# Kernel tuning notes

Hardware: AMD Instinct MI355X
Metric: run time of the kernel (lower is better)

Reference implementation:

```python
import jax, jax.numpy as jnp
import numpy as np

G = 8      # conv groups
NH = 8     # attention heads per group
B, HID, S = 4, 2048, 4096
OUT = 2048


def setup_inputs() -> dict:
    key = jax.random.key(0)
    k1, k2, k3 = jax.random.split(key, 3)
    dim = HID // G
    # xavier-uniform-like scales for conv1d(k=1) weights
    sc_qkv = (6.0 / (dim + 3 * HID // 1)) ** 0.5 * 0.5
    sc_pred = (6.0 / (dim + OUT)) ** 0.5 * 0.5
    return {
        "x": jax.random.normal(k1, (B, HID, S), dtype=jnp.float32),
        # torch weight [3*hid, dim, 1] -> per-group [G, 3*dim, dim]
        "w_qkv": jax.random.uniform(k2, (G, 3 * dim, dim), jnp.float32, -sc_qkv, sc_qkv),
        "b_qkv": jnp.zeros((G, 3 * dim), jnp.float32),
        # torch weight [out, dim, 1] -> per-group [G, out//G, dim]
        "w_pred": jax.random.uniform(k3, (G, OUT // G, dim), jnp.float32, -sc_pred, sc_pred),
        "b_pred": jnp.zeros((G, OUT // G), jnp.float32),
    }


def reference(x, w_qkv, b_qkv, w_pred, b_pred):
    Bb, Hd, Ss = x.shape
    dim = Hd // G
    dk = dim // NH
    # ConstantPad1d((0,1),0)
    xp = jnp.pad(x, ((0, 0), (0, 0), (0, 1)))            # [B, Hd, S+1]
    xg = xp.reshape(Bb, G, dim, Ss + 1)
    # grouped 1x1 conv: per-group GEMM dim -> 3*dim
    y = jnp.einsum('bgct,goc->bgot', xg, w_qkv) + b_qkv[None, :, :, None]
    y = y.reshape(Bb, G, dim, 3, Ss + 1)                 # qkv interleaved per channel
    q = y[..., 0, :-1]                                   # [B, G, dim, S]
    k = jnp.concatenate((y[..., 1, :-1], y[..., 1, 1:]), axis=1)  # [B, 2G, dim, S]
    v = jnp.concatenate((y[..., 2, :-1], y[..., 2, 1:]), axis=1)
    qr = q.reshape(Bb, G, NH, dk, Ss)
    kr = k.reshape(Bb, 2 * G, NH, dk, Ss)
    vr = v.reshape(Bb, 2 * G, NH, dk, Ss)
    # scores[b,n,s,g,e] = sum_d q[b,g,n,d,s] k[b,e,n,d,s] / sqrt(dk)
    scores = jnp.einsum('bgnds,bends->bnsge', qr, kr) * (dk ** -0.5)
    # normalized sigmoid over last axis (2G)
    z = jax.nn.sigmoid(scores)
    attn = z / (1e-9 + jnp.sum(z, axis=-1, keepdims=True))
    # out[b,g,n,d,s] = sum_e attn[b,n,s,g,e] v[b,e,n,d,s]
    out = jnp.einsum('bnsge,bends->bgnds', attn, vr).reshape(Bb, Hd, Ss)
    og = out.reshape(Bb, G, dim, Ss)
    pred = jnp.einsum('bgct,goc->bgot', og, w_pred) + b_pred[None, :, :, None]
    pred = pred.reshape(Bb, -1, Ss)                      # [B, OUT, S]
    attn_out = jnp.transpose(attn, (0, 1, 3, 4, 2))      # [B, NH, G, 2G, S]
    return pred, attn_out
```

## Files before the change

### kernel.cpp

```cpp
#include <hip/hip_runtime.h>
#include <math.h>

#define BQ   4
#define GQ   8
#define NHQ  8
#define SQ   4096


typedef __attribute__((ext_vector_type(8))) short short8;
typedef __attribute__((ext_vector_type(4))) float f32x4;

__device__ __forceinline__ unsigned short f2b(float f) {
    unsigned int u = __float_as_uint(f);
    unsigned int r = u + 0x7fffu + ((u >> 16) & 1u);
    return (unsigned short)(r >> 16);
}
__device__ __forceinline__ float b2f(unsigned short h) {
    return __uint_as_float(((unsigned int)h) << 16);
}
__device__ __forceinline__ void gll16(const void* g, void* l) {
    __builtin_amdgcn_global_load_lds((const __attribute__((address_space(1))) void*)g,
                                     (__attribute__((address_space(3))) void*)l, 16, 0, 0);
}

__global__ __launch_bounds__(256) void convert_x_k(const float* __restrict__ x,
    unsigned short* __restrict__ xhi, unsigned short* __restrict__ xlo)
{
    __shared__ float lds[64 * 65];
    const int tid = threadIdx.x;
    const int t0 = blockIdx.x << 6;
    const int c0 = blockIdx.y << 6;
    const int bg = blockIdx.z;
    const int hi16 = tid >> 4, lo16 = tid & 15;
    const float* xb = x + ((size_t)bg << 8) * SQ;
#pragma unroll
    for (int p = 0; p < 4; ++p) {
        int c = (p << 4) + hi16;
        const float4 v4 = *(const float4*)(xb + (size_t)(c0 + c) * SQ + t0 + (lo16 << 2));
        lds[((lo16 << 2) + 0) * 65 + c] = v4.x;
        lds[((lo16 << 2) + 1) * 65 + c] = v4.y;
        lds[((lo16 << 2) + 2) * 65 + c] = v4.z;
        lds[((lo16 << 2) + 3) * 65 + c] = v4.w;
    }
    __syncthreads();
#pragma unroll
    for (int p = 0; p < 4; ++p) {
        int t = (p << 4) + hi16;
        float f0 = lds[t * 65 + (lo16 << 2) + 0];
        float f1 = lds[t * 65 + (lo16 << 2) + 1];
        float f2 = lds[t * 65 + (lo16 << 2) + 2];
        float f3 = lds[t * 65 + (lo16 << 2) + 3];
        ushort4 h, l;
        h.x = f2b(f0); l.x = f2b(f0 - b2f(h.x));
        h.y = f2b(f1); l.y = f2b(f1 - b2f(h.y));
        h.z = f2b(f2); l.z = f2b(f2 - b2f(h.z));
        h.w = f2b(f3); l.w = f2b(f3 - b2f(h.w));
        size_t o = (((size_t)bg * SQ + t0 + t) << 8) + c0 + (lo16 << 2);
        *(ushort4*)(xhi + o) = h;
        *(ushort4*)(xlo + o) = l;
    }
}

template <int M, bool QKV>
__global__ __launch_bounds__(256) void gemm2_k(
    const float* __restrict__ W,
    const unsigned short* __restrict__ Bh, const unsigned short* __restrict__ Bl,
    const float* __restrict__ bias,
    float* __restrict__ o0p, float* __restrict__ o1p, float* __restrict__ o2p)
{
    __shared__ __align__(16) char smem[32768];
    const int AHI = 0, ALO = 8192, BHI = 16384, BLO = 24576;
    const int tid = threadIdx.x;
    const int lane = tid & 63, wid = tid >> 6;
    const int wm = wid >> 1, wn = wid & 1;
    const int o0 = blockIdx.x << 7;
    const int t0 = blockIdx.y << 7;
    const int bg = blockIdx.z;
    const int g = bg & 7;
    const float* Wg = W + (size_t)g * M * 256;
    const size_t brow0 = (((size_t)bg * SQ + t0) << 8);

    f32x4 acc[4][4];
    const f32x4 zero = {0.f, 0.f, 0.f, 0.f};
#pragma unroll
    for (int i = 0; i < 4; ++i)
#pragma unroll
        for (int j = 0; j < 4; ++j) acc[i][j] = zero;

    for (int k0 = 0; k0 < 256; k0 += 32) {
#pragma unroll
        for (int s = 0; s < 2; ++s) {
            int w = tid + (s << 8);
            int row = w >> 2;
            int j = (w & 3) ^ ((w >> 3) & 3);
            size_t go = brow0 + ((size_t)row << 8) + k0 + (j << 3);
            gll16(Bh + go, smem + BHI + (w << 4));
            gll16(Bl + go, smem + BLO + (w << 4));
        }
#pragma unroll
        for (int p = 0; p < 4; ++p) {
            int qd = tid + (p << 8);
            int row = qd >> 3, kq = qd & 7;
            const float4 a4 = *(const float4*)(Wg + (size_t)(o0 + row) * 256 + k0 + (kq << 2));
            ushort4 h, l;
            h.x = f2b(a4.x); l.x = f2b(a4.x - b2f(h.x));
            h.y = f2b(a4.y); l.y = f2b(a4.y - b2f(h.y));
            h.z = f2b(a4.z); l.z = f2b(a4.z - b2f(h.z));
            h.w = f2b(a4.w); l.w = f2b(a4.w - b2f(h.w));
            int base = (row << 6) + ((((kq >> 1) ^ ((row >> 1) & 3)) << 4)) + ((kq & 1) << 3);
            *(ushort4*)(smem + AHI + base) = h;
            *(ushort4*)(smem + ALO + base) = l;
        }
        __syncthreads();

        short8 ah[4], al[4], bh[4], bl[4];
        const int lr = lane & 15, kc = lane >> 4;
#pragma unroll
        for (int mi = 0; mi < 4; ++mi) {
            int row = (wm << 6) + (mi << 4) + lr;
            int off = (row << 6) + ((kc ^ ((row >> 1) & 3)) << 4);
            ah[mi] = *(const short8*)(smem + AHI + off);
            al[mi] = *(const short8*)(smem + ALO + off);
        }
#pragma unroll
        for (int ni = 0; ni < 4; ++ni) {
            int row = (wn << 6) + (ni << 4) + lr;
            int off = (row << 6) + ((kc ^ ((row >> 1) & 3)) << 4);
            bh[ni] = *(const short8*)(smem + BHI + off);
            bl[ni] = *(const short8*)(smem + BLO + off);
        }
#pragma unroll
        for (int mi = 0; mi < 4; ++mi)
#pragma unroll
            for (int ni = 0; ni < 4; ++ni)
                acc[mi][ni] = __builtin_amdgcn_mfma_f32_16x16x32_bf16(ah[mi], bh[ni], acc[mi][ni], 0, 0, 0);
#pragma unroll
        for (int mi = 0; mi < 4; ++mi)
#pragma unroll
            for (int ni = 0; ni < 4; ++ni)
                acc[mi][ni] = __builtin_amdgcn_mfma_f32_16x16x32_bf16(ah[mi], bl[ni], acc[mi][ni], 0, 0, 0);
#pragma unroll
        for (int mi = 0; mi < 4; ++mi)
#pragma unroll
            for (int ni = 0; ni < 4; ++ni)
                acc[mi][ni] = __builtin_amdgcn_mfma_f32_16x16x32_bf16(al[mi], bh[ni], acc[mi][ni], 0, 0, 0);
        __syncthreads();
    }

    const int lr = lane & 15, lq = lane >> 4;
#pragma unroll
    for (int mi = 0; mi < 4; ++mi) {
#pragma unroll
        for (int r = 0; r < 4; ++r) {
            const int row = o0 + (wm << 6) + (mi << 4) + (lq << 2) + r;
            const float bo = bias[g * M + row];
            float* rowbase;
            if (QKV) {
                const int j = row % 3, c = row / 3;
                float* bp = (j == 0) ? o0p : ((j == 1) ? o1p : o2p);
                rowbase = bp + (((size_t)bg * 256 + c) << 12);
            } else {
                rowbase = o0p + (((size_t)(bg >> 3) * 2048 + g * 256 + row) << 12);
            }
#pragma unroll
            for (int ni = 0; ni < 4; ++ni) {
                const int t = t0 + (wn << 6) + (ni << 4) + lr;
                rowbase[t] = acc[mi][ni][r] + bo;
            }
        }
    }
}

__global__ __launch_bounds__(256) void pad_k(const float* __restrict__ bqkv,
                                             float* __restrict__ kpad, float* __restrict__ vpad)
{
    int i = blockIdx.x * 256 + threadIdx.x;
    int c = i & 255;
    int g = (i >> 8) & 7;
    kpad[i] = bqkv[g * 768 + c * 3 + 1];
    vpad[i] = bqkv[g * 768 + c * 3 + 2];
}

__global__ __launch_bounds__(256) void attn_k(
    const float* __restrict__ q, const float* __restrict__ k, const float* __restrict__ v,
    const float* __restrict__ kpad, const float* __restrict__ vpad,
    unsigned short* __restrict__ oghi, unsigned short* __restrict__ oglo,
    float* __restrict__ aout)
{
    __shared__ float qo_s[4620];
    __shared__ float k_s[4607];
    __shared__ float v_s[4607];
    __shared__ float at_s[2182];

    const int tid = threadIdx.x;
    const int t0 = blockIdx.x << 4;
    const int n  = blockIdx.y;
    const int b  = blockIdx.z;

#pragma unroll
    for (int i = 0; i < 4; ++i) {
        int f = tid + (i << 8);
        int row = f >> 2, cq = f & 3;
        int d = row >> 3, g = row & 7;
        const float4 val = *(const float4*)(q + (((size_t)((b * GQ + g) * 256 + n * 32 + d)) << 12) + t0 + (cq << 2));
        float* lp = &qo_s[row * 18 + (cq << 2)];
        lp[0] = val.x; lp[1] = val.y; lp[2] = val.z; lp[3] = val.w;
    }
#pragma unroll
    for (int i = 0; i < 4; ++i) {
        int f = tid + (i << 8);
        int r = f >> 2, cq = f & 3;
        int d = r >> 3, e8 = r & 7;
        size_t gofs = (((size_t)((b * GQ + e8) * 256 + n * 32 + d)) << 12) + t0 + (cq << 2);
        const float4 k4 = *(const float4*)(k + gofs);
        float* lk = &k_s[(d * 8 + e8) * 18 + (cq << 2)];
        lk[0] = k4.x; lk[1] = k4.y; lk[2] = k4.z; lk[3] = k4.w;
        const float4 v4 = *(const float4*)(v + gofs);
        float* lv = &v_s[(e8 * 32 + d) * 18 + (cq << 2)];
        lv[0] = v4.x; lv[1] = v4.y; lv[2] = v4.z; lv[3] = v4.w;
    }
    {
        int r = tid;
        int d = r >> 3, e8 = r & 7;
        float kv, vv;
        if (t0 + 16 < SQ) {
            size_t gofs = (((size_t)((b * GQ + e8) * 256 + n * 32 + d)) << 12) + t0 + 16;
            kv = k[gofs]; vv = v[gofs];
        } else {
            int pi = (b * GQ + e8) * 256 + n * 32 + d;
            kv = kpad[pi]; vv = vpad[pi];
        }
        k_s[(d * 8 + e8) * 18 + 16] = kv;
        v_s[(e8 * 32 + d) * 18 + 16] = vv;
    }
    __syncthreads();

    {
        const int p = tid >> 7;
        const int idx = tid & 127;
        const int g = idx >> 4, e = idx & 15;
        const int e8 = e & 7, hi = e >> 3;
#pragma unroll
        for (int it = 0; it < 8; ++it) {
            const int t = (it << 1) + p;
            float s = 0.f;
#pragma unroll
            for (int d = 0; d < 32; ++d)
                s += qo_s[(d * 8 + g) * 18 + t] * k_s[(d * 8 + e8) * 18 + t + hi];
            s *= 0.17677669529663687f;
            const float z = 1.f / (1.f + __expf(-s));
            float zs = z;
#pragma unroll
            for (int off = 1; off < 16; off <<= 1)
                zs += __shfl_xor(zs, off);
            at_s[(g * 16 + e) * 17 + g + t] = z / (1e-9f + zs);
        }
    }
    __syncthreads();

    {
        const int p4 = tid >> 6;
        const int l = tid & 63;
        const int g = l >> 3, dq = l & 7;
#pragma unroll
        for (int it = 0; it < 4; ++it) {
            const int t = (it << 2) + p4;
            float a0 = 0.f, a1 = 0.f, a2 = 0.f, a3 = 0.f;
#pragma unroll
            for (int e = 0; e < 16; ++e) {
                const int e8 = e & 7, hi = e >> 3;
                const float a = at_s[(g * 16 + e) * 17 + g + t];
                const float* vp = &v_s[(e8 * 32 + (dq << 2)) * 18 + t + hi];
                a0 += a * vp[0 * 18];
                a1 += a * vp[1 * 18];
                a2 += a * vp[2 * 18];
                a3 += a * vp[3 * 18];
            }
            float* op = &qo_s[((g << 5) + (dq << 2)) * 18 + (g << 1) + t];
            op[0 * 18] = a0; op[1 * 18] = a1; op[2 * 18] = a2; op[3 * 18] = a3;
        }
    }
    __syncthreads();

#pragma unroll
    for (int i = 0; i < 4; ++i) {
        int f = tid + (i << 8);
        int row = f >> 3, t2 = f & 7;
        int gg = row >> 4;
        float x0 = at_s[row * 17 + gg + (t2 << 1)];
        float x1 = at_s[row * 17 + gg + (t2 << 1) + 1];
        float* gp = aout + (((size_t)((b * NHQ + n) * 128 + row)) << 12) + t0 + (t2 << 1);
        *(float2*)gp = make_float2(x0, x1);
    }
#pragma unroll
    for (int i = 0; i < 16; ++i) {
        int f = tid + (i << 8);
        int t = f >> 8, rc = f & 255;
        int gg = rc >> 5, d = rc & 31;
        float val = qo_s[rc * 18 + (gg << 1) + t];
        unsigned short hh = f2b(val);
        unsigned short ll = f2b(val - b2f(hh));
        size_t o = (((size_t)((b * GQ + gg) * SQ + t0 + t)) << 8) + n * 32 + d;
        oghi[o] = hh;
        oglo[o] = ll;
    }
}

extern "C" void kernel_launch(void* const* d_in, const int* in_sizes, int n_in,
                              void* d_out, int out_size, void* d_ws, size_t ws_size,
                              hipStream_t stream)
{
    const float* x      = (const float*)d_in[0];
    const float* w_qkv  = (const float*)d_in[1];
    const float* b_qkv  = (const float*)d_in[2];
    const float* w_pred = (const float*)d_in[3];
    const float* b_pred = (const float*)d_in[4];

    float* pred = (float*)d_out;
    float* aout = pred + (size_t)33554432;

    unsigned short* xt_hi = (unsigned short*)d_out;
    unsigned short* xt_lo = xt_hi + (size_t)33554432;
    float* kpad = (float*)d_out;
    float* vpad = kpad + 8192;

    float* q  = (float*)d_ws;
    float* kb = q + (size_t)33554432;
    float* vb = kb + (size_t)33554432;
    unsigned short* og_hi = (unsigned short*)(vb + (size_t)33554432);
    unsigned short* og_lo = og_hi + (size_t)33554432;

    convert_x_k<<<dim3(64, 4, 32), 256, 0, stream>>>(x, xt_hi, xt_lo);
    gemm2_k<768, true><<<dim3(6, 32, 32), 256, 0, stream>>>(w_qkv, xt_hi, xt_lo, b_qkv, q, kb, vb);
    pad_k<<<32, 256, 0, stream>>>(b_qkv, kpad, vpad);
    attn_k<<<dim3(SQ / 16, NHQ, BQ), 256, 0, stream>>>(q, kb, vb, kpad, vpad, og_hi, og_lo, aout);
    gemm2_k<256, false><<<dim3(2, 32, 32), 256, 0, stream>>>(w_pred, og_hi, og_lo, b_pred, pred, nullptr, nullptr);
}
```

Measured before the change: 860.6 us.

## Preconvert weights to bf16 split, swizzle GEMM grid, rewrite attention per-timestep

```diff
diff --git a/kernel.cpp b/kernel.cpp
--- a/kernel.cpp
+++ b/kernel.cpp
@@ -61,24 +61,46 @@
     }
 }
 
+__global__ __launch_bounds__(256) void convert_w_k(const float* __restrict__ W,
+    unsigned short* __restrict__ Wh, unsigned short* __restrict__ Wl, int n4)
+{
+    int i = blockIdx.x * 256 + threadIdx.x;
+    if (i >= n4) return;
+    const float4 w4 = ((const float4*)W)[i];
+    ushort4 h, l;
+    h.x = f2b(w4.x); l.x = f2b(w4.x - b2f(h.x));
+    h.y = f2b(w4.y); l.y = f2b(w4.y - b2f(h.y));
+    h.z = f2b(w4.z); l.z = f2b(w4.z - b2f(h.z));
+    h.w = f2b(w4.w); l.w = f2b(w4.w - b2f(h.w));
+    ((ushort4*)Wh)[i] = h;
+    ((ushort4*)Wl)[i] = l;
+}
+
 template <int M, bool QKV>
-__global__ __launch_bounds__(256) void gemm2_k(
-    const float* __restrict__ W,
+__global__ __launch_bounds__(256) void gemm3_k(
+    const unsigned short* __restrict__ Ah, const unsigned short* __restrict__ Al,
     const unsigned short* __restrict__ Bh, const unsigned short* __restrict__ Bl,
     const float* __restrict__ bias,
     float* __restrict__ o0p, float* __restrict__ o1p, float* __restrict__ o2p)
 {
+    constexpr int NO = M / 128;
     __shared__ __align__(16) char smem[32768];
     const int AHI = 0, ALO = 8192, BHI = 16384, BLO = 24576;
     const int tid = threadIdx.x;
     const int lane = tid & 63, wid = tid >> 6;
     const int wm = wid >> 1, wn = wid & 1;
-    const int o0 = blockIdx.x << 7;
-    const int t0 = blockIdx.y << 7;
-    const int bg = blockIdx.z;
+
+    const int nblk = gridDim.x;
+    const int lin = blockIdx.x;
+    const int L = (lin & 7) * (nblk >> 3) + (lin >> 3);
+    const int oi = L % NO;
+    const int r = L / NO;
+    const int t_idx = r & 31, bg = r >> 5;
+    const int o0 = oi << 7, t0 = t_idx << 7;
     const int g = bg & 7;
-    const float* Wg = W + (size_t)g * M * 256;
-    const size_t brow0 = (((size_t)bg * SQ + t0) << 8);
+
+    const size_t abase = (size_t)g * M * 256;
+    const size_t bbase = (((size_t)bg << 12) + (size_t)t0) << 8;
 
     f32x4 acc[4][4];
     const f32x4 zero = {0.f, 0.f, 0.f, 0.f};
@@ -93,23 +115,12 @@
             int w = tid + (s << 8);
             int row = w >> 2;
             int j = (w & 3) ^ ((w >> 3) & 3);
-            size_t go = brow0 + ((size_t)row << 8) + k0 + (j << 3);
-            gll16(Bh + go, smem + BHI + (w << 4));
-            gll16(Bl + go, smem + BLO + (w << 4));
-        }
-#pragma unroll
-        for (int p = 0; p < 4; ++p) {
-            int qd = tid + (p << 8);
-            int row = qd >> 3, kq = qd & 7;
-            const float4 a4 = *(const float4*)(Wg + (size_t)(o0 + row) * 256 + k0 + (kq << 2));
-            ushort4 h, l;
-            h.x = f2b(a4.x); l.x = f2b(a4.x - b2f(h.x));
-            h.y = f2b(a4.y); l.y = f2b(a4.y - b2f(h.y));
-            h.z = f2b(a4.z); l.z = f2b(a4.z - b2f(h.z));
-            h.w = f2b(a4.w); l.w = f2b(a4.w - b2f(h.w));
-            int base = (row << 6) + ((((kq >> 1) ^ ((row >> 1) & 3)) << 4)) + ((kq & 1) << 3);
-            *(ushort4*)(smem + AHI + base) = h;
-            *(ushort4*)(smem + ALO + base) = l;
+            size_t ga = abase + (size_t)(o0 + row) * 256 + k0 + (j << 3);
+            size_t gb = bbase + ((size_t)row << 8) + k0 + (j << 3);
+            gll16(Ah + ga, smem + AHI + (w << 4));
+            gll16(Al + ga, smem + ALO + (w << 4));
+            gll16(Bh + gb, smem + BHI + (w << 4));
+            gll16(Bl + gb, smem + BLO + (w << 4));
         }
         __syncthreads();
 
@@ -151,8 +162,8 @@
 #pragma unroll
     for (int mi = 0; mi < 4; ++mi) {
 #pragma unroll
-        for (int r = 0; r < 4; ++r) {
-            const int row = o0 + (wm << 6) + (mi << 4) + (lq << 2) + r;
+        for (int r2 = 0; r2 < 4; ++r2) {
+            const int row = o0 + (wm << 6) + (mi << 4) + (lq << 2) + r2;
             const float bo = bias[g * M + row];
             float* rowbase;
             if (QKV) {
@@ -165,144 +176,121 @@
 #pragma unroll
             for (int ni = 0; ni < 4; ++ni) {
                 const int t = t0 + (wn << 6) + (ni << 4) + lr;
-                rowbase[t] = acc[mi][ni][r] + bo;
+                rowbase[t] = acc[mi][ni][r2] + bo;
             }
         }
     }
 }
 
-__global__ __launch_bounds__(256) void pad_k(const float* __restrict__ bqkv,
-                                             float* __restrict__ kpad, float* __restrict__ vpad)
-{
-    int i = blockIdx.x * 256 + threadIdx.x;
-    int c = i & 255;
-    int g = (i >> 8) & 7;
-    kpad[i] = bqkv[g * 768 + c * 3 + 1];
-    vpad[i] = bqkv[g * 768 + c * 3 + 2];
-}
-
-__global__ __launch_bounds__(256) void attn_k(
-    const float* __restrict__ q, const float* __restrict__ k, const float* __restrict__ v,
-    const float* __restrict__ kpad, const float* __restrict__ vpad,
-    unsigned short* __restrict__ oghi, unsigned short* __restrict__ oglo,
+__global__ __launch_bounds__(512) void attn2_k(
+    const float* __restrict__ q, const float* __restrict__ kb, const float* __restrict__ vb,
+    const float* __restrict__ bqkv,
+    unsigned short* __restrict__ og_h, unsigned short* __restrict__ og_l,
     float* __restrict__ aout)
 {
-    __shared__ float qo_s[4620];
-    __shared__ float k_s[4607];
-    __shared__ float v_s[4607];
-    __shared__ float at_s[2182];
-
-    const int tid = threadIdx.x;
-    const int t0 = blockIdx.x << 4;
-    const int n  = blockIdx.y;
-    const int b  = blockIdx.z;
-
-#pragma unroll
-    for (int i = 0; i < 4; ++i) {
-        int f = tid + (i << 8);
-        int row = f >> 2, cq = f & 3;
-        int d = row >> 3, g = row & 7;
-        const float4 val = *(const float4*)(q + (((size_t)((b * GQ + g) * 256 + n * 32 + d)) << 12) + t0 + (cq << 2));
-        float* lp = &qo_s[row * 18 + (cq << 2)];
-        lp[0] = val.x; lp[1] = val.y; lp[2] = val.z; lp[3] = val.w;
-    }
-#pragma unroll
-    for (int i = 0; i < 4; ++i) {
-        int f = tid + (i << 8);
-        int r = f >> 2, cq = f & 3;
-        int d = r >> 3, e8 = r & 7;
-        size_t gofs = (((size_t)((b * GQ + e8) * 256 + n * 32 + d)) << 12) + t0 + (cq << 2);
-        const float4 k4 = *(const float4*)(k + gofs);
-        float* lk = &k_s[(d * 8 + e8) * 18 + (cq << 2)];
-        lk[0] = k4.x; lk[1] = k4.y; lk[2] = k4.z; lk[3] = k4.w;
-        const float4 v4 = *(const float4*)(v + gofs);
-        float* lv = &v_s[(e8 * 32 + d) * 18 + (cq << 2)];
-        lv[0] = v4.x; lv[1] = v4.y; lv[2] = v4.z; lv[3] = v4.w;
-    }
+    __shared__ unsigned int ogt[64 * 256];
+
+    const int nblk = gridDim.x;
+    const int lin = blockIdx.x;
+    const int L = (lin & 7) * (nblk >> 3) + (lin >> 3);
+    const int g = L & 7;
+    const int tt = (L >> 3) & 63;
+    const int b = L >> 9;
+    const int t0 = tt << 6;
+    const int n = threadIdx.x >> 6;
+    const int tl = (int)threadIdx.x & 63;
+    const int t = t0 + tl;
+    const bool lastblk = (t0 == SQ - 64);
+
+    const int b8 = b << 3;
+    const float* qrow = q + (((size_t)((b8 + g) << 8) + (n << 5)) << 12);
+    const float* krow = kb + (((size_t)(b8 << 8) + (n << 5)) << 12);
+    const float* vrow = vb + (((size_t)(b8 << 8) + (n << 5)) << 12);
+
+    float s[16];
+#pragma unroll
+    for (int e = 0; e < 16; ++e) s[e] = 0.f;
+
+#pragma unroll 4
+    for (int d = 0; d < 32; ++d) {
+        const float qv = qrow[((size_t)d << 12) + t];
+#pragma unroll
+        for (int e8 = 0; e8 < 8; ++e8) {
+            const float* kr = krow + ((size_t)((e8 << 8) + d) << 12);
+            s[e8]     += qv * kr[t];
+            s[8 + e8] += qv * kr[t + 1];
+        }
+    }
+    if (lastblk) {
+        if (t == SQ - 1) {
+#pragma unroll
+            for (int e8 = 0; e8 < 8; ++e8) s[8 + e8] = 0.f;
+            for (int d = 0; d < 32; ++d) {
+                const float qv = qrow[((size_t)d << 12) + t];
+#pragma unroll
+                for (int e8 = 0; e8 < 8; ++e8)
+                    s[8 + e8] += qv * bqkv[e8 * 768 + ((n << 5) + d) * 3 + 1];
+            }
+        }
+    }
+
+    float zs = 0.f;
+#pragma unroll
+    for (int e = 0; e < 16; ++e) {
+        const float z = 1.f / (1.f + __expf(-s[e] * 0.17677669529663687f));
+        s[e] = z; zs += z;
+    }
+    const float inv = 1.f / (1e-9f + zs);
+#pragma unroll
+    for (int e = 0; e < 16; ++e) s[e] *= inv;
+
     {
-        int r = tid;
-        int d = r >> 3, e8 = r & 7;
-        float kv, vv;
-        if (t0 + 16 < SQ) {
-            size_t gofs = (((size_t)((b * GQ + e8) * 256 + n * 32 + d)) << 12) + t0 + 16;
-            kv = k[gofs]; vv = v[gofs];
-        } else {
-            int pi = (b * GQ + e8) * 256 + n * 32 + d;
-            kv = kpad[pi]; vv = vpad[pi];
-        }
-        k_s[(d * 8 + e8) * 18 + 16] = kv;
-        v_s[(e8 * 32 + d) * 18 + 16] = vv;
+        const size_t abase = ((size_t)(((b * NHQ + n) * GQ + g) << 4) << 12) + t;
+#pragma unroll
+        for (int e = 0; e < 16; ++e)
+            aout[abase + ((size_t)e << 12)] = s[e];
+    }
+
+    for (int d = 0; d < 32; ++d) {
+        float v0k[8];
+        float acc = 0.f;
+#pragma unroll
+        for (int e8 = 0; e8 < 8; ++e8) {
+            const float* vr = vrow + ((size_t)((e8 << 8) + d) << 12);
+            const float v0 = vr[t];
+            const float v1 = vr[t + 1];
+            v0k[e8] = v0;
+            acc += s[e8] * v0 + s[8 + e8] * v1;
+        }
+        if (lastblk) {
+            if (t == SQ - 1) {
+                acc = 0.f;
+#pragma unroll
+                for (int e8 = 0; e8 < 8; ++e8)
+                    acc += s[e8] * v0k[e8] + s[8 + e8] * bqkv[e8 * 768 + ((n << 5) + d) * 3 + 2];
+            }
+        }
+        const unsigned short hh = f2b(acc);
+        const unsigned short ll = f2b(acc - b2f(hh));
+        const int c = (n << 5) + d;
+        ogt[(tl << 8) + (c ^ (tl & 31))] = ((unsigned)hh << 16) | (unsigned)ll;
     }
     __syncthreads();
 
-    {
-        const int p = tid >> 7;
-        const int idx = tid & 127;
-        const int g = idx >> 4, e = idx & 15;
-        const int e8 = e & 7, hi = e >> 3;
-#pragma unroll
-        for (int it = 0; it < 8; ++it) {
-            const int t = (it << 1) + p;
-            float s = 0.f;
-#pragma unroll
-            for (int d = 0; d < 32; ++d)
-                s += qo_s[(d * 8 + g) * 18 + t] * k_s[(d * 8 + e8) * 18 + t + hi];
-            s *= 0.17677669529663687f;
-            const float z = 1.f / (1.f + __expf(-s));
-            float zs = z;
-#pragma unroll
-            for (int off = 1; off < 16; off <<= 1)
-                zs += __shfl_xor(zs, off);
-            at_s[(g * 16 + e) * 17 + g + t] = z / (1e-9f + zs);
-        }
-    }
-    __syncthreads();
-
-    {
-        const int p4 = tid >> 6;
-        const int l = tid & 63;
-        const int g = l >> 3, dq = l & 7;
-#pragma unroll
-        for (int it = 0; it < 4; ++it) {
-            const int t = (it << 2) + p4;
-            float a0 = 0.f, a1 = 0.f, a2 = 0.f, a3 = 0.f;
-#pragma unroll
-            for (int e = 0; e < 16; ++e) {
-                const int e8 = e & 7, hi = e >> 3;
-                const float a = at_s[(g * 16 + e) * 17 + g + t];
-                const float* vp = &v_s[(e8 * 32 + (dq << 2)) * 18 + t + hi];
-                a0 += a * vp[0 * 18];
-                a1 += a * vp[1 * 18];
-                a2 += a * vp[2 * 18];
-                a3 += a * vp[3 * 18];
-            }
-            float* op = &qo_s[((g << 5) + (dq << 2)) * 18 + (g << 1) + t];
-            op[0 * 18] = a0; op[1 * 18] = a1; op[2 * 18] = a2; op[3 * 18] = a3;
-        }
-    }
-    __syncthreads();
-
-#pragma unroll
-    for (int i = 0; i < 4; ++i) {
-        int f = tid + (i << 8);
-        int row = f >> 3, t2 = f & 7;
-        int gg = row >> 4;
-        float x0 = at_s[row * 17 + gg + (t2 << 1)];
-        float x1 = at_s[row * 17 + gg + (t2 << 1) + 1];
-        float* gp = aout + (((size_t)((b * NHQ + n) * 128 + row)) << 12) + t0 + (t2 << 1);
-        *(float2*)gp = make_float2(x0, x1);
-    }
-#pragma unroll
-    for (int i = 0; i < 16; ++i) {
-        int f = tid + (i << 8);
-        int t = f >> 8, rc = f & 255;
-        int gg = rc >> 5, d = rc & 31;
-        float val = qo_s[rc * 18 + (gg << 1) + t];
-        unsigned short hh = f2b(val);
-        unsigned short ll = f2b(val - b2f(hh));
-        size_t o = (((size_t)((b * GQ + gg) * SQ + t0 + t)) << 8) + n * 32 + d;
-        oghi[o] = hh;
-        oglo[o] = ll;
+    const size_t rb = ((size_t)(b8 + g) << 12) + t0;
+#pragma unroll
+    for (int it = 0; it < 16; ++it) {
+        const int qq = (int)threadIdx.x + (it << 9);
+        const int trow = qq >> 7;
+        const int cp = (qq & 127) << 1;
+        const unsigned u0 = ogt[(trow << 8) + (cp ^ (trow & 31))];
+        const unsigned u1 = ogt[(trow << 8) + ((cp + 1) ^ (trow & 31))];
+        const size_t off = ((rb + trow) << 8) + cp;
+        ushort2 hv, lv;
+        hv.x = (unsigned short)(u0 >> 16); hv.y = (unsigned short)(u1 >> 16);
+        lv.x = (unsigned short)(u0 & 0xffffu); lv.y = (unsigned short)(u1 & 0xffffu);
+        *(ushort2*)(og_h + off) = hv;
+        *(ushort2*)(og_l + off) = lv;
     }
 }
 
@@ -319,20 +307,23 @@
     float* pred = (float*)d_out;
     float* aout = pred + (size_t)33554432;
 
-    unsigned short* xt_hi = (unsigned short*)d_out;
-    unsigned short* xt_lo = xt_hi + (size_t)33554432;
-    float* kpad = (float*)d_out;
-    float* vpad = kpad + 8192;
+    unsigned short* xt_h = (unsigned short*)d_out;
+    unsigned short* xt_l = xt_h + (size_t)33554432;
+    unsigned short* Wq_h = (unsigned short*)aout;
+    unsigned short* Wq_l = Wq_h + (size_t)1572864;
 
     float* q  = (float*)d_ws;
     float* kb = q + (size_t)33554432;
     float* vb = kb + (size_t)33554432;
-    unsigned short* og_hi = (unsigned short*)(vb + (size_t)33554432);
-    unsigned short* og_lo = og_hi + (size_t)33554432;
-
-    convert_x_k<<<dim3(64, 4, 32), 256, 0, stream>>>(x, xt_hi, xt_lo);
-    gemm2_k<768, true><<<dim3(6, 32, 32), 256, 0, stream>>>(w_qkv, xt_hi, xt_lo, b_qkv, q, kb, vb);
-    pad_k<<<32, 256, 0, stream>>>(b_qkv, kpad, vpad);
-    attn_k<<<dim3(SQ / 16, NHQ, BQ), 256, 0, stream>>>(q, kb, vb, kpad, vpad, og_hi, og_lo, aout);
-    gemm2_k<256, false><<<dim3(2, 32, 32), 256, 0, stream>>>(w_pred, og_hi, og_lo, b_pred, pred, nullptr, nullptr);
-}
+    unsigned short* og_h = (unsigned short*)(vb + (size_t)33554432);
+    unsigned short* og_l = og_h + (size_t)33554432;
+    unsigned short* Wp_h = (unsigned short*)d_ws;
+    unsigned short* Wp_l = Wp_h + (size_t)524288;
+
+    convert_x_k<<<dim3(64, 4, 32), 256, 0, stream>>>(x, xt_h, xt_l);
+    convert_w_k<<<1536, 256, 0, stream>>>(w_qkv, Wq_h, Wq_l, 393216);
+    gemm3_k<768, true><<<6144, 256, 0, stream>>>(Wq_h, Wq_l, xt_h, xt_l, b_qkv, q, kb, vb);
+    attn2_k<<<2048, 512, 0, stream>>>(q, kb, vb, b_qkv, og_h, og_l, aout);
+    convert_w_k<<<512, 256, 0, stream>>>(w_pred, Wp_h, Wp_l, 131072);
+    gemm3_k<256, false><<<2048, 256, 0, stream>>>(Wp_h, Wp_l, og_h, og_l, b_pred, pred, nullptr, nullptr);
+}
```

Result: slower. 1.035 ms (+20.3%).
